# Kernel optimization log

Measured on AMD Instinct MI355X. Metric: run time of the kernel, lower is better.

Reference implementation:

```python
import jax, jax.numpy as jnp
import numpy as np

N, D = 8192, 512


def _l2norm(x):
    return x / jnp.linalg.norm(x, axis=-1, keepdims=True)


def setup_inputs() -> dict:
    key = jax.random.key(0)
    k1, k2 = jax.random.split(key)
    image_features = _l2norm(jax.random.normal(k1, (N, D), dtype=jnp.float32))
    text_features = _l2norm(jax.random.normal(k2, (N, D), dtype=jnp.float32))
    logit_scale = jnp.asarray(100.0, dtype=jnp.float32)  # exp(4.6), standard CLIP temperature
    return {"image_features": image_features, "text_features": text_features, "logit_scale": logit_scale}


def reference(image_features, text_features, logit_scale):
    # logits_per_image = scale * img @ txt.T ; logits_per_text is its transpose (world_size=1)
    logits = logit_scale * (image_features @ text_features.T)  # [N, N]
    n = logits.shape[0]
    idx = jnp.arange(n)
    # CE with labels = arange(N): loss = -mean(diag(log_softmax(logits)))
    lse_row = jax.nn.logsumexp(logits, axis=1)  # for logits_per_image
    lse_col = jax.nn.logsumexp(logits, axis=0)  # for logits_per_text = logits.T
    diag = logits[idx, idx]
    loss_i = jnp.mean(lse_row - diag)
    loss_t = jnp.mean(lse_col - diag)
    contrastive_loss = (loss_i + loss_t) / 2
    return contrastive_loss
```

## Files before the change

kernel.cpp:

```cpp
#include <hip/hip_runtime.h>
#include <stdint.h>

#define N_ROWS 8192
#define DDIM   512

typedef __bf16 bf16_t;
typedef bf16_t bf16x8 __attribute__((ext_vector_type(8)));
typedef float  f32x4  __attribute__((ext_vector_type(4)));

__device__ inline uint16_t f2bf(float f) {
    uint32_t u = __float_as_uint(f);
    u += 0x7FFFu + ((u >> 16) & 1u);
    return (uint16_t)(u >> 16);
}

__global__ void convert_bf16(const float* __restrict__ a, const float* __restrict__ b,
                             uint16_t* __restrict__ abf, uint16_t* __restrict__ bbf) {
    const int quads = N_ROWS * DDIM / 4;
    const int stride = gridDim.x * blockDim.x;
    for (int i = blockIdx.x * blockDim.x + threadIdx.x; i < quads; i += stride) {
        float4 va = ((const float4*)a)[i];
        float4 vb = ((const float4*)b)[i];
        ushort4 ra, rb;
        ra.x = f2bf(va.x); ra.y = f2bf(va.y); ra.z = f2bf(va.z); ra.w = f2bf(va.w);
        rb.x = f2bf(vb.x); rb.y = f2bf(vb.y); rb.z = f2bf(vb.z); rb.w = f2bf(vb.w);
        ((ushort4*)abf)[i] = ra;
        ((ushort4*)bbf)[i] = rb;
    }
}

__device__ inline void stage16(const uint8_t* g, uint8_t* lds_wave_base) {
#if __has_builtin(__builtin_amdgcn_global_load_lds)
    __builtin_amdgcn_global_load_lds(
        (const __attribute__((address_space(1))) uint32_t*)g,
        (__attribute__((address_space(3))) uint32_t*)lds_wave_base, 16, 0, 0);
#else
    *(int4*)(lds_wave_base) = *(const int4*)g;
#endif
}

__global__ void __launch_bounds__(256)
clip_gemm(const uint16_t* __restrict__ A, const uint16_t* __restrict__ B,
          const float* __restrict__ scale_p,
          float* __restrict__ rowsum, float* __restrict__ colsum,
          float* __restrict__ diag) {
    __shared__ __attribute__((aligned(16))) uint8_t As[128 * 64];
    __shared__ __attribute__((aligned(16))) uint8_t Bs[128 * 64];

    const int t    = threadIdx.x;
    const int wave = t >> 6;
    const int lane = t & 63;
    const int wr   = wave >> 1;
    const int wc   = wave & 1;
    const int bm   = blockIdx.x;
    const int bn   = blockIdx.y;

    const float s     = *scale_p;
    const float shift = s - 64.0f;

    f32x4 acc[4][4];
#pragma unroll
    for (int m = 0; m < 4; ++m)
#pragma unroll
        for (int n = 0; n < 4; ++n)
#pragma unroll
            for (int r = 0; r < 4; ++r) acc[m][n][r] = 0.0f;

    const size_t rowbytes = (size_t)DDIM * 2;
    const int    kchunk   = ((t & 3) ^ ((t >> 2) & 3)) * 16;
    const uint8_t* Ag = (const uint8_t*)A + (size_t)(bm * 128 + (t >> 2)) * rowbytes + kchunk;
    const uint8_t* Bg = (const uint8_t*)B + (size_t)(bn * 128 + (t >> 2)) * rowbytes + kchunk;
    const size_t rowskip = (size_t)64 * rowbytes;

    uint8_t* AsW = As + wave * 1024;
    uint8_t* BsW = Bs + wave * 1024;

    const int lr = lane & 15;
    const int lg = lane >> 4;
    const int rq = ((lg ^ (lane & 3)) * 16);

    for (int k0 = 0; k0 < DDIM; k0 += 32) {
        __syncthreads();
        const size_t kb = (size_t)k0 * 2;
        stage16(Ag + kb,           AsW);
        stage16(Ag + kb + rowskip, AsW + 4096);
        stage16(Bg + kb,           BsW);
        stage16(Bg + kb + rowskip, BsW + 4096);
        __syncthreads();

        bf16x8 a[4], b[4];
#pragma unroll
        for (int m = 0; m < 4; ++m)
            a[m] = *(const bf16x8*)(As + (wr * 64 + m * 16 + lr) * 64 + rq);
#pragma unroll
        for (int n = 0; n < 4; ++n)
            b[n] = *(const bf16x8*)(Bs + (wc * 64 + n * 16 + lr) * 64 + rq);
#pragma unroll
        for (int m = 0; m < 4; ++m)
#pragma unroll
            for (int n = 0; n < 4; ++n)
                acc[m][n] = __builtin_amdgcn_mfma_f32_16x16x32_bf16(a[m], b[n], acc[m][n], 0, 0, 0);
    }

    float rpart[4][4];
    float cpart[4] = {0.f, 0.f, 0.f, 0.f};
#pragma unroll
    for (int m = 0; m < 4; ++m)
#pragma unroll
        for (int r = 0; r < 4; ++r) rpart[m][r] = 0.f;

#pragma unroll
    for (int m = 0; m < 4; ++m) {
#pragma unroll
        for (int n = 0; n < 4; ++n) {
#pragma unroll
            for (int r = 0; r < 4; ++r) {
                const float logit = s * acc[m][n][r];
                const float e = __expf(logit - shift);
                rpart[m][r] += e;
                cpart[n]    += e;
                if (bm == bn && wr == wc && m == n && lr == lg * 4 + r)
                    diag[bm * 128 + wr * 64 + m * 16 + lr] = logit;
            }
        }
    }

#pragma unroll
    for (int m = 0; m < 4; ++m) {
#pragma unroll
        for (int r = 0; r < 4; ++r) {
            float v = rpart[m][r];
            v += __shfl_xor(v, 1);
            v += __shfl_xor(v, 2);
            v += __shfl_xor(v, 4);
            v += __shfl_xor(v, 8);
            if (lr == 0)
                atomicAdd(&rowsum[bm * 128 + wr * 64 + m * 16 + lg * 4 + r], v);
        }
    }
#pragma unroll
    for (int n = 0; n < 4; ++n) {
        float v = cpart[n];
        v += __shfl_xor(v, 16);
        v += __shfl_xor(v, 32);
        if (lg == 0)
            atomicAdd(&colsum[bn * 128 + wc * 64 + n * 16 + lr], v);
    }
}

__global__ void clip_finalize(const float* __restrict__ rowsum, const float* __restrict__ colsum,
                              const float* __restrict__ diag, const float* __restrict__ scale_p,
                              float* __restrict__ out) {
    __shared__ float red[4];
    const float s = *scale_p;
    const float shift = s - 64.0f;
    const int i = blockIdx.x * 256 + threadIdx.x;
    float acc = logf(rowsum[i]) + logf(colsum[i]) + 2.f * shift - 2.f * diag[i];
#pragma unroll
    for (int m = 1; m < 64; m <<= 1) acc += __shfl_xor(acc, m);
    const int wave = threadIdx.x >> 6;
    const int lane = threadIdx.x & 63;
    if (lane == 0) red[wave] = acc;
    __syncthreads();
    if (threadIdx.x == 0) {
        atomicAdd(out, (red[0] + red[1] + red[2] + red[3]) / (2.0f * N_ROWS));
    }
}

extern "C" void kernel_launch(void* const* d_in, const int* in_sizes, int n_in,
                              void* d_out, int out_size, void* d_ws, size_t ws_size,
                              hipStream_t stream) {
    const float* img     = (const float*)d_in[0];
    const float* txt     = (const float*)d_in[1];
    const float* scale_p = (const float*)d_in[2];

    uint8_t* ws = (uint8_t*)d_ws;
    uint16_t* Abf   = (uint16_t*)ws;
    uint16_t* Bbf   = (uint16_t*)(ws + (size_t)8 * 1024 * 1024);
    float*    rowsum = (float*)(ws + (size_t)16 * 1024 * 1024);
    float*    colsum = rowsum + N_ROWS;
    float*    diag   = colsum + N_ROWS;
    float*    out    = (float*)d_out;

    hipMemsetAsync(rowsum, 0, 2 * N_ROWS * sizeof(float), stream);
    hipMemsetAsync(out, 0, sizeof(float), stream);
    convert_bf16<<<1024, 256, 0, stream>>>(img, txt, Abf, Bbf);
    dim3 grid(64, 64);
    clip_gemm<<<grid, 256, 0, stream>>>(Abf, Bbf, scale_p, rowsum, colsum, diag);
    clip_finalize<<<32, 256, 0, stream>>>(rowsum, colsum, diag, scale_p, out);
}
```

Before: 127.5 us.

## Enlarge GEMM tile to 256x256 with double-buffered async staging and XCD-aware block mapping

Replaces the 128x128 tile, single-buffered GEMM with a 256x256 tile computed by 8 waves. It uses 128 KB of LDS double-buffered over a K-step of 64, with direct global-to-LDS staging and vmcnt-based waits. MFMA work is interleaved with LDS fragment loads under s_setprio, and block IDs are remapped so neighbouring tiles share an XCD. The intent is to cut global/LDS traffic per FLOP and overlap loads with compute, at the cost of heavy register and LDS use and a fragile hand-written barrier schedule.

```diff
diff --git a/kernel.cpp b/kernel.cpp
--- a/kernel.cpp
+++ b/kernel.cpp
@@ -7,6 +7,8 @@
 typedef __bf16 bf16_t;
 typedef bf16_t bf16x8 __attribute__((ext_vector_type(8)));
 typedef float  f32x4  __attribute__((ext_vector_type(4)));
+
+#define MFMA_BF16 __builtin_amdgcn_mfma_f32_16x16x32_bf16
 
 __device__ inline uint16_t f2bf(float f) {
     uint32_t u = __float_as_uint(f);
@@ -39,112 +41,184 @@
 #endif
 }
 
-__global__ void __launch_bounds__(256)
+__global__ void __launch_bounds__(512, 2)
 clip_gemm(const uint16_t* __restrict__ A, const uint16_t* __restrict__ B,
           const float* __restrict__ scale_p,
           float* __restrict__ rowsum, float* __restrict__ colsum,
           float* __restrict__ diag) {
-    __shared__ __attribute__((aligned(16))) uint8_t As[128 * 64];
-    __shared__ __attribute__((aligned(16))) uint8_t Bs[128 * 64];
+    __shared__ __attribute__((aligned(16))) uint8_t sh[131072];
 
     const int t    = threadIdx.x;
     const int wave = t >> 6;
     const int lane = t & 63;
-    const int wr   = wave >> 1;
-    const int wc   = wave & 1;
-    const int bm   = blockIdx.x;
-    const int bn   = blockIdx.y;
+    const int wm   = wave >> 2;
+    const int wn   = wave & 3;
+    const int lr   = lane & 15;
+    const int lg   = lane >> 4;
+
+    const int orig = blockIdx.x;
+    const int wg   = (orig & 7) * 128 + (orig >> 3);
+    const int bm   = wg >> 5;
+    const int bn   = wg & 31;
 
     const float s     = *scale_p;
     const float shift = s - 64.0f;
 
-    f32x4 acc[4][4];
-#pragma unroll
-    for (int m = 0; m < 4; ++m)
-#pragma unroll
-        for (int n = 0; n < 4; ++n)
-#pragma unroll
-            for (int r = 0; r < 4; ++r) acc[m][n][r] = 0.0f;
-
-    const size_t rowbytes = (size_t)DDIM * 2;
-    const int    kchunk   = ((t & 3) ^ ((t >> 2) & 3)) * 16;
-    const uint8_t* Ag = (const uint8_t*)A + (size_t)(bm * 128 + (t >> 2)) * rowbytes + kchunk;
-    const uint8_t* Bg = (const uint8_t*)B + (size_t)(bn * 128 + (t >> 2)) * rowbytes + kchunk;
-    const size_t rowskip = (size_t)64 * rowbytes;
-
-    uint8_t* AsW = As + wave * 1024;
-    uint8_t* BsW = Bs + wave * 1024;
-
-    const int lr = lane & 15;
-    const int lg = lane >> 4;
-    const int rq = ((lg ^ (lane & 3)) * 16);
-
-    for (int k0 = 0; k0 < DDIM; k0 += 32) {
-        __syncthreads();
-        const size_t kb = (size_t)k0 * 2;
-        stage16(Ag + kb,           AsW);
-        stage16(Ag + kb + rowskip, AsW + 4096);
-        stage16(Bg + kb,           BsW);
-        stage16(Bg + kb + rowskip, BsW + 4096);
-        __syncthreads();
-
-        bf16x8 a[4], b[4];
-#pragma unroll
-        for (int m = 0; m < 4; ++m)
-            a[m] = *(const bf16x8*)(As + (wr * 64 + m * 16 + lr) * 64 + rq);
-#pragma unroll
-        for (int n = 0; n < 4; ++n)
-            b[n] = *(const bf16x8*)(Bs + (wc * 64 + n * 16 + lr) * 64 + rq);
-#pragma unroll
-        for (int m = 0; m < 4; ++m)
-#pragma unroll
-            for (int n = 0; n < 4; ++n)
-                acc[m][n] = __builtin_amdgcn_mfma_f32_16x16x32_bf16(a[m], b[n], acc[m][n], 0, 0, 0);
-    }
-
-    float rpart[4][4];
-    float cpart[4] = {0.f, 0.f, 0.f, 0.f};
-#pragma unroll
-    for (int m = 0; m < 4; ++m)
-#pragma unroll
-        for (int r = 0; r < 4; ++r) rpart[m][r] = 0.f;
-
-#pragma unroll
-    for (int m = 0; m < 4; ++m) {
-#pragma unroll
-        for (int n = 0; n < 4; ++n) {
+    f32x4 acc[8][4];
+#pragma unroll
+    for (int i = 0; i < 8; ++i)
+#pragma unroll
+        for (int j = 0; j < 4; ++j)
+#pragma unroll
+            for (int r = 0; r < 4; ++r) acc[i][j][r] = 0.0f;
+
+    const int g16 = (((t & 7) ^ ((t >> 3) & 7)) << 4);
+    const uint8_t* srcA = (const uint8_t*)A + (size_t)(bm * 256 + (t >> 3)) * 1024 + g16;
+    const uint8_t* srcB = (const uint8_t*)B + (size_t)(bn * 256 + (t >> 3)) * 1024 + g16;
+    uint8_t* dA = sh + wave * 1024;
+    uint8_t* dB = sh + 32768 + wave * 1024;
+
+#define STAGE_TILE(kt, bsel) do {                                              \
+        const size_t ko = (size_t)(kt) * 128;                                  \
+        _Pragma("unroll")                                                      \
+        for (int c = 0; c < 4; ++c) {                                          \
+            stage16(srcA + ko + (size_t)c * 65536, dA + (bsel) * 65536 + c * 8192); \
+            stage16(srcB + ko + (size_t)c * 65536, dB + (bsel) * 65536 + c * 8192); \
+        }                                                                      \
+    } while (0)
+
+    const int x0   = ((lg) ^ (lane & 7)) << 4;
+    const int x1   = ((4 | lg) ^ (lane & 7)) << 4;
+    const int aoff = (wm * 128 + lr) * 128;
+    const int boff = 32768 + (wn * 64 + lr) * 128;
+
+    STAGE_TILE(0, 0);
+    STAGE_TILE(1, 1);
+    asm volatile("s_waitcnt vmcnt(8)" ::: "memory");
+    __builtin_amdgcn_s_barrier();
+
+    for (int tt = 0; tt < 8; ++tt) {
+        const uint8_t* base = sh + (tt & 1) * 65536;
+        const uint8_t* pA0 = base + aoff + x0;
+        const uint8_t* pA1 = base + aoff + x1;
+        const uint8_t* pB0 = base + boff + x0;
+        const uint8_t* pB1 = base + boff + x1;
+
+        bf16x8 a[4][2], b[4][2];
+
+#pragma unroll
+        for (int i = 0; i < 4; ++i) {
+            a[i][0] = *(const bf16x8*)(pA0 + i * 2048);
+            a[i][1] = *(const bf16x8*)(pA1 + i * 2048);
+        }
+#pragma unroll
+        for (int j = 0; j < 2; ++j) {
+            b[j][0] = *(const bf16x8*)(pB0 + j * 2048);
+            b[j][1] = *(const bf16x8*)(pB1 + j * 2048);
+        }
+        __builtin_amdgcn_s_barrier();
+        __builtin_amdgcn_s_setprio(1);
+#pragma unroll
+        for (int i = 0; i < 4; ++i)
+#pragma unroll
+            for (int j = 0; j < 2; ++j) {
+                acc[i][j] = MFMA_BF16(a[i][0], b[j][0], acc[i][j], 0, 0, 0);
+                acc[i][j] = MFMA_BF16(a[i][1], b[j][1], acc[i][j], 0, 0, 0);
+            }
+        __builtin_amdgcn_s_setprio(0);
+        __builtin_amdgcn_s_barrier();
+
+#pragma unroll
+        for (int j = 2; j < 4; ++j) {
+            b[j][0] = *(const bf16x8*)(pB0 + j * 2048);
+            b[j][1] = *(const bf16x8*)(pB1 + j * 2048);
+        }
+        __builtin_amdgcn_s_barrier();
+        __builtin_amdgcn_s_setprio(1);
+#pragma unroll
+        for (int i = 0; i < 4; ++i)
+#pragma unroll
+            for (int j = 2; j < 4; ++j) {
+                acc[i][j] = MFMA_BF16(a[i][0], b[j][0], acc[i][j], 0, 0, 0);
+                acc[i][j] = MFMA_BF16(a[i][1], b[j][1], acc[i][j], 0, 0, 0);
+            }
+        __builtin_amdgcn_s_setprio(0);
+        __builtin_amdgcn_s_barrier();
+
+#pragma unroll
+        for (int i = 0; i < 4; ++i) {
+            a[i][0] = *(const bf16x8*)(pA0 + 8192 + i * 2048);
+            a[i][1] = *(const bf16x8*)(pA1 + 8192 + i * 2048);
+        }
+        __builtin_amdgcn_s_barrier();
+        __builtin_amdgcn_s_setprio(1);
+#pragma unroll
+        for (int i = 0; i < 4; ++i)
+#pragma unroll
+            for (int j = 0; j < 2; ++j) {
+                acc[4 + i][j] = MFMA_BF16(a[i][0], b[j][0], acc[4 + i][j], 0, 0, 0);
+                acc[4 + i][j] = MFMA_BF16(a[i][1], b[j][1], acc[4 + i][j], 0, 0, 0);
+            }
+        __builtin_amdgcn_s_setprio(0);
+        __builtin_amdgcn_s_barrier();
+
+        if (tt < 6) STAGE_TILE(tt + 2, tt & 1);
+        __builtin_amdgcn_s_setprio(1);
+#pragma unroll
+        for (int i = 0; i < 4; ++i)
+#pragma unroll
+            for (int j = 2; j < 4; ++j) {
+                acc[4 + i][j] = MFMA_BF16(a[i][0], b[j][0], acc[4 + i][j], 0, 0, 0);
+                acc[4 + i][j] = MFMA_BF16(a[i][1], b[j][1], acc[4 + i][j], 0, 0, 0);
+            }
+        __builtin_amdgcn_s_setprio(0);
+        if (tt < 6) {
+            asm volatile("s_waitcnt vmcnt(8)" ::: "memory");
+            __builtin_amdgcn_s_barrier();
+        } else if (tt == 6) {
+            asm volatile("s_waitcnt vmcnt(0)" ::: "memory");
+            __builtin_amdgcn_s_barrier();
+        }
+    }
+#undef STAGE_TILE
+
+    float cp[4] = {0.f, 0.f, 0.f, 0.f};
+#pragma unroll
+    for (int i = 0; i < 8; ++i) {
+        float rp[4] = {0.f, 0.f, 0.f, 0.f};
+#pragma unroll
+        for (int j = 0; j < 4; ++j) {
 #pragma unroll
             for (int r = 0; r < 4; ++r) {
-                const float logit = s * acc[m][n][r];
+                const float logit = s * acc[i][j][r];
                 const float e = __expf(logit - shift);
-                rpart[m][r] += e;
-                cpart[n]    += e;
-                if (bm == bn && wr == wc && m == n && lr == lg * 4 + r)
-                    diag[bm * 128 + wr * 64 + m * 16 + lr] = logit;
-            }
-        }
-    }
-
-#pragma unroll
-    for (int m = 0; m < 4; ++m) {
+                rp[r] += e;
+                cp[j] += e;
+                if (bm == bn) {
+                    const int rr = wm * 128 + i * 16 + lg * 4 + r;
+                    const int cc = wn * 64 + j * 16 + lr;
+                    if (rr == cc) diag[bm * 256 + rr] = logit;
+                }
+            }
+        }
 #pragma unroll
         for (int r = 0; r < 4; ++r) {
-            float v = rpart[m][r];
+            float v = rp[r];
             v += __shfl_xor(v, 1);
             v += __shfl_xor(v, 2);
             v += __shfl_xor(v, 4);
             v += __shfl_xor(v, 8);
             if (lr == 0)
-                atomicAdd(&rowsum[bm * 128 + wr * 64 + m * 16 + lg * 4 + r], v);
-        }
-    }
-#pragma unroll
-    for (int n = 0; n < 4; ++n) {
-        float v = cpart[n];
+                atomicAdd(&rowsum[bm * 256 + wm * 128 + i * 16 + lg * 4 + r], v);
+        }
+    }
+#pragma unroll
+    for (int j = 0; j < 4; ++j) {
+        float v = cp[j];
         v += __shfl_xor(v, 16);
         v += __shfl_xor(v, 32);
         if (lg == 0)
-            atomicAdd(&colsum[bn * 128 + wc * 64 + n * 16 + lr], v);
+            atomicAdd(&colsum[bn * 256 + wn * 64 + j * 16 + lr], v);
     }
 }
 
@@ -185,7 +259,6 @@
     hipMemsetAsync(rowsum, 0, 2 * N_ROWS * sizeof(float), stream);
     hipMemsetAsync(out, 0, sizeof(float), stream);
     convert_bf16<<<1024, 256, 0, stream>>>(img, txt, Abf, Bbf);
-    dim3 grid(64, 64);
-    clip_gemm<<<grid, 256, 0, stream>>>(Abf, Bbf, scale_p, rowsum, colsum, diag);
+    clip_gemm<<<1024, 512, 0, stream>>>(Abf, Bbf, scale_p, rowsum, colsum, diag);
     clip_finalize<<<32, 256, 0, stream>>>(rowsum, colsum, diag, scale_p, out);
 }
```

New measurement: 166.5 us. 30.6% more time.

## Use 256x256 tiles with 32x32 MFMA, double-buffered LDS and XCD-aware block mapping

Applied to the files above, without the earlier changes.

Replaces the 128x128 single-buffered GEMM tile with a 256x256 tile per 512-thread block, using 32x32x16 bf16 MFMA instructions. Each k-step stages 128 bytes of K into a double-buffered 128KB LDS region with an XOR swizzle, and uses manual vmcnt waits and register double-buffering of fragments to overlap global loads with compute. Block IDs are remapped so each XCD handles a localized group of tiles for L2 reuse. Because one block uses 128KB of LDS, occupancy is limited, and the larger accumulator footprint raises register pressure.

```diff
diff --git a/kernel.cpp b/kernel.cpp
--- a/kernel.cpp
+++ b/kernel.cpp
@@ -6,7 +6,9 @@
 
 typedef __bf16 bf16_t;
 typedef bf16_t bf16x8 __attribute__((ext_vector_type(8)));
-typedef float  f32x4  __attribute__((ext_vector_type(4)));
+typedef float  f32x16 __attribute__((ext_vector_type(16)));
+
+#define MFMA32 __builtin_amdgcn_mfma_f32_32x32x16_bf16
 
 __device__ inline uint16_t f2bf(float f) {
     uint32_t u = __float_as_uint(f);
@@ -39,112 +41,159 @@
 #endif
 }
 
-__global__ void __launch_bounds__(256)
+__global__ void __launch_bounds__(512, 2)
 clip_gemm(const uint16_t* __restrict__ A, const uint16_t* __restrict__ B,
           const float* __restrict__ scale_p,
           float* __restrict__ rowsum, float* __restrict__ colsum,
           float* __restrict__ diag) {
-    __shared__ __attribute__((aligned(16))) uint8_t As[128 * 64];
-    __shared__ __attribute__((aligned(16))) uint8_t Bs[128 * 64];
+    __shared__ __attribute__((aligned(16))) uint8_t sh[131072];
 
     const int t    = threadIdx.x;
     const int wave = t >> 6;
     const int lane = t & 63;
-    const int wr   = wave >> 1;
-    const int wc   = wave & 1;
-    const int bm   = blockIdx.x;
-    const int bn   = blockIdx.y;
+    const int wm   = wave >> 2;
+    const int wn   = wave & 3;
+    const int l31  = lane & 31;
+    const int hl   = lane >> 5;
+    const int l7   = lane & 7;
+
+    const int orig = blockIdx.x;
+    const int xcd  = orig & 7;
+    const int idx  = orig >> 3;
+    const int bm   = (xcd & 3) * 8  + (idx & 7);
+    const int bn   = (xcd >> 2) * 16 + (idx >> 3);
 
     const float s     = *scale_p;
     const float shift = s - 64.0f;
 
-    f32x4 acc[4][4];
-#pragma unroll
-    for (int m = 0; m < 4; ++m)
-#pragma unroll
-        for (int n = 0; n < 4; ++n)
-#pragma unroll
-            for (int r = 0; r < 4; ++r) acc[m][n][r] = 0.0f;
-
-    const size_t rowbytes = (size_t)DDIM * 2;
-    const int    kchunk   = ((t & 3) ^ ((t >> 2) & 3)) * 16;
-    const uint8_t* Ag = (const uint8_t*)A + (size_t)(bm * 128 + (t >> 2)) * rowbytes + kchunk;
-    const uint8_t* Bg = (const uint8_t*)B + (size_t)(bn * 128 + (t >> 2)) * rowbytes + kchunk;
-    const size_t rowskip = (size_t)64 * rowbytes;
-
-    uint8_t* AsW = As + wave * 1024;
-    uint8_t* BsW = Bs + wave * 1024;
-
-    const int lr = lane & 15;
-    const int lg = lane >> 4;
-    const int rq = ((lg ^ (lane & 3)) * 16);
-
-    for (int k0 = 0; k0 < DDIM; k0 += 32) {
-        __syncthreads();
-        const size_t kb = (size_t)k0 * 2;
-        stage16(Ag + kb,           AsW);
-        stage16(Ag + kb + rowskip, AsW + 4096);
-        stage16(Bg + kb,           BsW);
-        stage16(Bg + kb + rowskip, BsW + 4096);
-        __syncthreads();
-
-        bf16x8 a[4], b[4];
-#pragma unroll
-        for (int m = 0; m < 4; ++m)
-            a[m] = *(const bf16x8*)(As + (wr * 64 + m * 16 + lr) * 64 + rq);
-#pragma unroll
-        for (int n = 0; n < 4; ++n)
-            b[n] = *(const bf16x8*)(Bs + (wc * 64 + n * 16 + lr) * 64 + rq);
-#pragma unroll
-        for (int m = 0; m < 4; ++m)
-#pragma unroll
-            for (int n = 0; n < 4; ++n)
-                acc[m][n] = __builtin_amdgcn_mfma_f32_16x16x32_bf16(a[m], b[n], acc[m][n], 0, 0, 0);
-    }
-
-    float rpart[4][4];
-    float cpart[4] = {0.f, 0.f, 0.f, 0.f};
-#pragma unroll
-    for (int m = 0; m < 4; ++m)
-#pragma unroll
-        for (int r = 0; r < 4; ++r) rpart[m][r] = 0.f;
-
-#pragma unroll
-    for (int m = 0; m < 4; ++m) {
-#pragma unroll
-        for (int n = 0; n < 4; ++n) {
-#pragma unroll
-            for (int r = 0; r < 4; ++r) {
-                const float logit = s * acc[m][n][r];
-                const float e = __expf(logit - shift);
-                rpart[m][r] += e;
-                cpart[n]    += e;
-                if (bm == bn && wr == wc && m == n && lr == lg * 4 + r)
-                    diag[bm * 128 + wr * 64 + m * 16 + lr] = logit;
-            }
+    f32x16 acc[4][2];
+#pragma unroll
+    for (int mi = 0; mi < 4; ++mi)
+#pragma unroll
+        for (int nj = 0; nj < 2; ++nj)
+#pragma unroll
+            for (int q = 0; q < 16; ++q) acc[mi][nj][q] = 0.0f;
+
+    const int g16 = (((t & 7) ^ ((t >> 3) & 7)) << 4);
+    const uint8_t* srcA = (const uint8_t*)A + (size_t)(bm * 256 + (t >> 3)) * 1024 + g16;
+    const uint8_t* srcB = (const uint8_t*)B + (size_t)(bn * 256 + (t >> 3)) * 1024 + g16;
+    uint8_t* dA = sh + wave * 1024;
+    uint8_t* dB = sh + 32768 + wave * 1024;
+
+#define STAGE8(kt, bsel) do {                                                   \
+        _Pragma("unroll")                                                       \
+        for (int c = 0; c < 4; ++c) {                                           \
+            stage16(srcA + (size_t)(kt) * 128 + (size_t)c * 65536,              \
+                    dA + (bsel) * 65536 + c * 8192);                            \
+            stage16(srcB + (size_t)(kt) * 128 + (size_t)c * 65536,              \
+                    dB + (bsel) * 65536 + c * 8192);                            \
+        }                                                                       \
+    } while (0)
+
+    const int aRow = (wm * 128 + l31) * 128;
+    const int bRow = 32768 + (wn * 64 + l31) * 128;
+
+#define LOADF(A0, A1, A2, A3, B0, B1, BASE, KK) do {                            \
+        const uint8_t* _b = (BASE);                                             \
+        const int _cx = ((((KK) * 2) + hl) ^ l7) << 4;                          \
+        A0 = *(const bf16x8*)(_b + aRow + 0 * 4096 + _cx);                      \
+        A1 = *(const bf16x8*)(_b + aRow + 1 * 4096 + _cx);                      \
+        A2 = *(const bf16x8*)(_b + aRow + 2 * 4096 + _cx);                      \
+        A3 = *(const bf16x8*)(_b + aRow + 3 * 4096 + _cx);                      \
+        B0 = *(const bf16x8*)(_b + bRow + 0 * 4096 + _cx);                      \
+        B1 = *(const bf16x8*)(_b + bRow + 1 * 4096 + _cx);                      \
+    } while (0)
+
+#define MMA8(A0, A1, A2, A3, B0, B1) do {                                       \
+        acc[0][0] = MFMA32(A0, B0, acc[0][0], 0, 0, 0);                         \
+        acc[0][1] = MFMA32(A0, B1, acc[0][1], 0, 0, 0);                         \
+        acc[1][0] = MFMA32(A1, B0, acc[1][0], 0, 0, 0);                         \
+        acc[1][1] = MFMA32(A1, B1, acc[1][1], 0, 0, 0);                         \
+        acc[2][0] = MFMA32(A2, B0, acc[2][0], 0, 0, 0);                         \
+        acc[2][1] = MFMA32(A2, B1, acc[2][1], 0, 0, 0);                         \
+        acc[3][0] = MFMA32(A3, B0, acc[3][0], 0, 0, 0);                         \
+        acc[3][1] = MFMA32(A3, B1, acc[3][1], 0, 0, 0);                         \
+    } while (0)
+
+    STAGE8(0, 0);
+    STAGE8(1, 1);
+    asm volatile("s_waitcnt vmcnt(8)" ::: "memory");
+    __builtin_amdgcn_s_barrier();
+
+    bf16x8 aC0, aC1, aC2, aC3, bC0, bC1;
+    bf16x8 aN0, aN1, aN2, aN3, bN0, bN1;
+    LOADF(aC0, aC1, aC2, aC3, bC0, bC1, sh, 0);
+
+    for (int tt = 0; tt < 8; ++tt) {
+        const uint8_t* base  = sh + (tt & 1) * 65536;
+        const uint8_t* obase = sh + ((tt + 1) & 1) * 65536;
+
+        LOADF(aN0, aN1, aN2, aN3, bN0, bN1, base, 1);
+        MMA8(aC0, aC1, aC2, aC3, bC0, bC1);
+        LOADF(aC0, aC1, aC2, aC3, bC0, bC1, base, 2);
+        MMA8(aN0, aN1, aN2, aN3, bN0, bN1);
+        LOADF(aN0, aN1, aN2, aN3, bN0, bN1, base, 3);
+        MMA8(aC0, aC1, aC2, aC3, bC0, bC1);
+
+        asm volatile("s_waitcnt vmcnt(0)" ::: "memory");
+        __builtin_amdgcn_s_barrier();
+
+        if (tt < 6) STAGE8(tt + 2, tt & 1);
+        if (tt < 7) LOADF(aC0, aC1, aC2, aC3, bC0, bC1, obase, 0);
+        MMA8(aN0, aN1, aN2, aN3, bN0, bN1);
+    }
+#undef STAGE8
+#undef LOADF
+#undef MMA8
+
+    float cp0 = 0.f, cp1 = 0.f;
+#pragma unroll
+    for (int mi = 0; mi < 4; ++mi) {
+        float rp[16];
+#pragma unroll
+        for (int q = 0; q < 16; ++q) rp[q] = 0.f;
+#pragma unroll
+        for (int q = 0; q < 16; ++q) {
+            const float l0 = s * acc[mi][0][q];
+            const float l1 = s * acc[mi][1][q];
+            const float e0 = __expf(l0 - shift);
+            const float e1 = __expf(l1 - shift);
+            rp[q] = e0 + e1;
+            cp0 += e0;
+            cp1 += e1;
         }
-    }
-
-#pragma unroll
-    for (int m = 0; m < 4; ++m) {
-#pragma unroll
-        for (int r = 0; r < 4; ++r) {
-            float v = rpart[m][r];
+#pragma unroll
+        for (int q = 0; q < 16; ++q) {
+            float v = rp[q];
             v += __shfl_xor(v, 1);
             v += __shfl_xor(v, 2);
             v += __shfl_xor(v, 4);
             v += __shfl_xor(v, 8);
-            if (lr == 0)
-                atomicAdd(&rowsum[bm * 128 + wr * 64 + m * 16 + lg * 4 + r], v);
+            v += __shfl_xor(v, 16);
+            if (l31 == 0) {
+                const int rr = wm * 128 + mi * 32 + (q & 3) + 8 * (q >> 2) + 4 * hl;
+                atomicAdd(&rowsum[bm * 256 + rr], v);
+            }
         }
     }
-#pragma unroll
-    for (int n = 0; n < 4; ++n) {
-        float v = cpart[n];
-        v += __shfl_xor(v, 16);
-        v += __shfl_xor(v, 32);
-        if (lg == 0)
-            atomicAdd(&colsum[bn * 128 + wc * 64 + n * 16 + lr], v);
+    cp0 += __shfl_xor(cp0, 32);
+    cp1 += __shfl_xor(cp1, 32);
+    if (hl == 0) {
+        atomicAdd(&colsum[bn * 256 + wn * 64 + l31], cp0);
+        atomicAdd(&colsum[bn * 256 + wn * 64 + 32 + l31], cp1);
+    }
+    if (bm == bn) {
+#pragma unroll
+        for (int mi = 0; mi < 4; ++mi)
+#pragma unroll
+            for (int nj = 0; nj < 2; ++nj)
+#pragma unroll
+                for (int q = 0; q < 16; ++q) {
+                    const int rr = wm * 128 + mi * 32 + (q & 3) + 8 * (q >> 2) + 4 * hl;
+                    const int cc = wn * 64 + nj * 32 + l31;
+                    if (rr == cc)
+                        diag[bm * 256 + rr] = s * acc[mi][nj][q];
+                }
     }
 }
 
@@ -185,7 +234,6 @@
     hipMemsetAsync(rowsum, 0, 2 * N_ROWS * sizeof(float), stream);
     hipMemsetAsync(out, 0, sizeof(float), stream);
     convert_bf16<<<1024, 256, 0, stream>>>(img, txt, Abf, Bbf);
-    dim3 grid(64, 64);
-    clip_gemm<<<grid, 256, 0, stream>>>(Abf, Bbf, scale_p, rowsum, colsum, diag);
+    clip_gemm<<<1024, 512, 0, stream>>>(Abf, Bbf, scale_p, rowsum, colsum, diag);
     clip_finalize<<<32, 256, 0, stream>>>(rowsum, colsum, diag, scale_p, out);
 }
```

Result: slower. 134.5 us (+5.5%).
